# Kernel tuning notes

Hardware: AMD Instinct MI355X
Metric: run time of the kernel (lower is better)

Reference implementation:

```python
import jax, jax.numpy as jnp
import numpy as np


def setup_inputs() -> dict:
    key = jax.random.key(0)
    ks = jax.random.split(key, 12)
    B, S, D = 2, 1024, 1024       # batch, seq_len, hidden
    DF_S, DF_E, E = 2048, 512, 8   # shared ffn, expert ffn, n_experts
    W = 0.02                       # weight init scale
    x = jax.random.normal(ks[0], (B, S, D), jnp.float32)
    router_weight = jax.random.normal(ks[1], (E, D), jnp.float32) * W
    sh_gate_w = jax.random.normal(ks[2], (DF_S, D), jnp.float32) * W
    sh_up_w = jax.random.normal(ks[3], (DF_S, D), jnp.float32) * W
    sh_down_w = jax.random.normal(ks[4], (D, DF_S), jnp.float32) * W
    gate_q = jax.random.randint(ks[5], (E, DF_E, D), -128, 128, jnp.int32)
    up_q = jax.random.randint(ks[6], (E, DF_E, D), -128, 128, jnp.int32)
    down_q = jax.random.randint(ks[7], (E, D, DF_E), -128, 128, jnp.int32)
    gate_s = jax.random.uniform(ks[8], (E, DF_E), jnp.float32) * 0.001
    up_s = jax.random.uniform(ks[9], (E, DF_E), jnp.float32) * 0.001
    down_s = jax.random.uniform(ks[10], (E, D), jnp.float32) * 0.001
    alpha = 0.5 + jax.random.uniform(ks[11], (E,), jnp.float32)  # effective_alpha per expert
    return dict(x=x, router_weight=router_weight, sh_gate_w=sh_gate_w,
                sh_up_w=sh_up_w, sh_down_w=sh_down_w, gate_s=gate_s,
                up_s=up_s, down_s=down_s, alpha=alpha, gate_q=gate_q,
                up_q=up_q, down_q=down_q, top_k=2)


def reference(x, router_weight, sh_gate_w, sh_up_w, sh_down_w,
              gate_s, up_s, down_s, alpha, gate_q, up_q, down_q, top_k):
    B, S, D = x.shape
    T = B * S
    E = router_weight.shape[0]
    xf = x.reshape(T, D).astype(jnp.float32)
    # shared SwiGLU MLP
    shared = (jax.nn.silu(xf @ sh_gate_w.T) * (xf @ sh_up_w.T)) @ sh_down_w.T  # [T, D]
    # router: top-k + softmax over selected logits
    logits = xf @ router_weight.T                                # [T, E]
    k = min(int(top_k), E)
    vals, idx = jax.lax.top_k(logits, k)
    w = jax.nn.softmax(vals, axis=-1)                            # [T, k]
    # scatter routing weights into dense combine matrix [T, E] (topk idx are distinct)
    combine = jnp.zeros((T, E), jnp.float32).at[jnp.arange(T)[:, None], idx].add(w)
    # on-the-fly dequantization: int8-range quants * per-row scale
    gw = gate_q.astype(jnp.float32) * gate_s[..., None]          # [E, DF_E, D]
    uw = up_q.astype(jnp.float32) * up_s[..., None]              # [E, DF_E, D]
    dw = down_q.astype(jnp.float32) * down_s[..., None]          # [E, D, DF_E]
    # expert SwiGLU for every (token, expert) pair, combined by routing weights
    g = jnp.einsum('td,efd->tef', xf, gw)                        # [T, E, DF_E]
    u = jnp.einsum('td,efd->tef', xf, uw)
    eo = jnp.einsum('tef,edf->ted', jax.nn.silu(g) * u, dw)      # [T, E, D]
    delta = eo - shared[:, None, :]                              # expert output minus shared
    mixed = shared + jnp.einsum('te,ted->td', combine * alpha[None, :], delta)
    return mixed.reshape(B, S, D)
```

## Files before the change

kernel.cpp:

```cpp
#include <hip/hip_runtime.h>
#include <math.h>

#define T_TOK 2048
#define D_DIM 1024
#define E_NUM 8
#define DFS   2048
#define DFE   512

#define BK 32

typedef short short8 __attribute__((ext_vector_type(8)));
typedef float floatx4 __attribute__((ext_vector_type(4)));
typedef unsigned short ushort;

__device__ __forceinline__ ushort f2b(float f) {
  union { float f; unsigned u; } v; v.f = f;
  unsigned r = (v.u + 0x7fffu + ((v.u >> 16) & 1u)) >> 16;
  return (ushort)r;
}

__device__ __forceinline__ void gld16(const ushort* g, ushort* l) {
  __builtin_amdgcn_global_load_lds(
      (const __attribute__((address_space(1))) void*)g,
      (__attribute__((address_space(3))) void*)l,
      16, 0, 0);
}

__device__ __forceinline__ float silu_mul(float g, float u) {
  return (g / (1.f + __expf(-g))) * u;
}

__global__ __launch_bounds__(256) void mega_prep(
    const float* __restrict__ x, const float* __restrict__ rw,
    const float* __restrict__ alpha,
    const float* __restrict__ sg, const float* __restrict__ su,
    const float* __restrict__ sd,
    const int* __restrict__ gq, const int* __restrict__ uq,
    const int* __restrict__ dq,
    int* __restrict__ choice, float2* __restrict__ cpair,
    float* __restrict__ csum, ushort* __restrict__ xb,
    ushort* __restrict__ sgb, ushort* __restrict__ subb,
    ushort* __restrict__ sdb,
    ushort* __restrict__ gqb, ushort* __restrict__ uqb,
    ushort* __restrict__ dqb) {
  const int b = blockIdx.x;
  const int tid = threadIdx.x;
  if (b < 512) {
    __shared__ float xs[4 * D_DIM];
    const size_t base = (size_t)b * 4 * D_DIM;
#pragma unroll
    for (int j = 0; j < 4; ++j) {
      const int idx = j * 1024 + tid * 4;
      float4 v = *(const float4*)(x + base + idx);
      *(float4*)&xs[idx] = v;
      union { ushort u[4]; uint2 p; } o;
      o.u[0] = f2b(v.x); o.u[1] = f2b(v.y); o.u[2] = f2b(v.z); o.u[3] = f2b(v.w);
      *(uint2*)(xb + base + idx) = o.p;
    }
    __syncthreads();
    const int w = tid >> 6, l = tid & 63;
    const int t = b * 4 + w;
    const int e = l >> 3, sub = l & 7;
    const float* wr = rw + e * D_DIM;
    float acc = 0.f;
#pragma unroll
    for (int k = 0; k < 32; ++k) {
      const int d = k * 32 + sub * 4;
      float4 xv = *(const float4*)&xs[w * D_DIM + d];
      float4 wv = *(const float4*)(wr + d);
      acc += xv.x * wv.x + xv.y * wv.y + xv.z * wv.z + xv.w * wv.w;
    }
    acc += __shfl_xor(acc, 1);
    acc += __shfl_xor(acc, 2);
    acc += __shfl_xor(acc, 4);
    float lg[8];
#pragma unroll
    for (int i = 0; i < 8; ++i) lg[i] = __shfl(acc, i * 8);
    if (l == 0) {
      int i0 = 0; float v0 = lg[0];
#pragma unroll
      for (int i = 1; i < E_NUM; ++i) if (lg[i] > v0) { v0 = lg[i]; i0 = i; }
      int i1 = -1; float v1 = -1e30f;
#pragma unroll
      for (int i = 0; i < E_NUM; ++i) {
        if (i == i0) continue;
        if (lg[i] > v1) { v1 = lg[i]; i1 = i; }
      }
      float w0 = 1.f / (1.f + __expf(v1 - v0));
      float w1 = 1.f - w0;
      float c0 = w0 * alpha[i0];
      float c1 = w1 * alpha[i1];
      csum[t] = c0 + c1;
      choice[t] = i0 | (i1 << 4);
      cpair[t] = make_float2(c0, c1);
    }
  } else if (b < 512 + 3072) {
    const int bb = b - 512;
    const int which = bb >> 10;
    const float* src; ushort* dst;
    if (which == 0) { src = sg; dst = sgb; }
    else if (which == 1) { src = su; dst = subb; }
    else { src = sd; dst = sdb; }
    const size_t i = (size_t)(bb & 1023) * 256 + tid;
    const float4* sp = (const float4*)src;
    float4 a = sp[2 * i], c = sp[2 * i + 1];
    union { ushort u[8]; uint4 v; } o;
    o.u[0] = f2b(a.x); o.u[1] = f2b(a.y); o.u[2] = f2b(a.z); o.u[3] = f2b(a.w);
    o.u[4] = f2b(c.x); o.u[5] = f2b(c.y); o.u[6] = f2b(c.z); o.u[7] = f2b(c.w);
    ((uint4*)dst)[i] = o.v;
  } else {
    const int bb = b - 3584;
    const int which = bb >> 11;
    const int* src; ushort* dst;
    if (which == 0) { src = gq; dst = gqb; }
    else if (which == 1) { src = uq; dst = uqb; }
    else { src = dq; dst = dqb; }
    const size_t i = (size_t)(bb & 2047) * 256 + tid;
    const int4* sp = (const int4*)src;
    int4 a = sp[2 * i], c = sp[2 * i + 1];
    union { ushort u[8]; uint4 v; } o;
    o.u[0] = f2b((float)a.x); o.u[1] = f2b((float)a.y);
    o.u[2] = f2b((float)a.z); o.u[3] = f2b((float)a.w);
    o.u[4] = f2b((float)c.x); o.u[5] = f2b((float)c.y);
    o.u[6] = f2b((float)c.z); o.u[7] = f2b((float)c.w);
    ((uint4*)dst)[i] = o.v;
  }
}

__global__ __launch_bounds__(1024) void build_lists(
    const int* __restrict__ choice, int* __restrict__ cnt,
    int* __restrict__ tok_list, uint2* __restrict__ ass) {
  __shared__ int lcnt[E_NUM];
  __shared__ int lbase[E_NUM];
  const int tid = threadIdx.x;
  if (tid < E_NUM) lcnt[tid] = 0;
  __syncthreads();
  uint2 tmp[T_TOK / 1024];
#pragma unroll
  for (int r = 0; r < T_TOK / 1024; ++r) {
    const int t = r * 1024 + tid;
    const int ch = choice[t];
    const int i0 = ch & 15, i1 = ch >> 4;
    const int p0 = atomicAdd(&lcnt[i0], 1);
    tok_list[i0 * T_TOK + p0] = t;
    const int p1 = atomicAdd(&lcnt[i1], 1);
    tok_list[i1 * T_TOK + p1] = t;
    tmp[r] = make_uint2((unsigned)((i0 << 16) | p0), (unsigned)((i1 << 16) | p1));
  }
  __syncthreads();
  if (tid < E_NUM) {
    int b = 0;
    for (int i = 0; i < tid; ++i) b += lcnt[i];
    lbase[tid] = b;
    cnt[tid] = lcnt[tid];
    cnt[8 + tid] = b;
  }
  __syncthreads();
#pragma unroll
  for (int r = 0; r < T_TOK / 1024; ++r) {
    const int t = r * 1024 + tid;
    const uint2 v = tmp[r];
    ass[t] = make_uint2(lbase[v.x >> 16] + (v.x & 0xffffu),
                        lbase[v.y >> 16] + (v.y & 0xffffu));
  }
}

#define SZGU (256 * BK)

__global__ __launch_bounds__(256) void mfma_gateup_all(
    const ushort* __restrict__ xb,
    const ushort* __restrict__ wg, const ushort* __restrict__ wu,
    const ushort* __restrict__ gq, const ushort* __restrict__ uq,
    const float* __restrict__ gate_s, const float* __restrict__ up_s,
    const int* __restrict__ cnt, const int* __restrict__ tok_list,
    ushort* __restrict__ sbuf, ushort* __restrict__ act) {
  const int bid = blockIdx.x;
  const bool is_sh = (bid < 512);
  const int tid = threadIdx.x;
  const int wave = tid >> 6, lane = tid & 63;
  const int wr = wave >> 1, wc = wave & 1;
  const int srow = lane >> 2;
  const int scol = (((lane & 3) ^ ((lane >> 3) & 3)) * 8);
  const int K = D_DIM;

  int m0, n0, e = 0, ce = 0, ebase = 0;
  const ushort *aR0, *aR1, *g0, *u0;
  if (is_sh) {
    n0 = (bid & 31) * 64;
    m0 = (bid >> 5) * 128;
    aR0 = xb + (size_t)(m0 + wave * 16 + srow) * K + scol;
    aR1 = aR0 + (size_t)64 * K;
    g0 = wg + (size_t)(n0 + wave * 16 + srow) * K + scol;
    u0 = wu + (size_t)(n0 + wave * 16 + srow) * K + scol;
  } else {
    const int r = bid - 512;
    e = r >> 7;
    const int rr = r & 127;
    n0 = (rr & 7) * 64;
    m0 = (rr >> 3) * 128;
    ce = cnt[e];
    if (m0 >= ce) return;
    ebase = cnt[8 + e];
    const int r0 = m0 + wave * 16 + srow;
    const int r1 = r0 + 64;
    const int tk0 = (r0 < ce) ? tok_list[e * T_TOK + r0] : 0;
    const int tk1 = (r1 < ce) ? tok_list[e * T_TOK + r1] : 0;
    aR0 = xb + (size_t)tk0 * K + scol;
    aR1 = xb + (size_t)tk1 * K + scol;
    g0 = gq + (size_t)e * DFE * D_DIM + (size_t)(n0 + wave * 16 + srow) * K + scol;
    u0 = uq + (size_t)e * DFE * D_DIM + (size_t)(n0 + wave * 16 + srow) * K + scol;
  }

  __shared__ ushort L[3 * SZGU];
  const int woff = (wave * 16) * BK;

  floatx4 accg[4][2], accu[4][2];
#pragma unroll
  for (int i = 0; i < 4; ++i)
#pragma unroll
    for (int j = 0; j < 2; ++j) { accg[i][j] = (floatx4)(0.f); accu[i][j] = (floatx4)(0.f); }

  const int kc = (((lane >> 4) ^ ((lane >> 1) & 3)) * 8);
  const int rb = lane & 15;
  const ushort* dA = &L[(wr * 64 + rb) * BK + kc];
  const ushort* dG = &L[128 * BK + (wc * 32 + rb) * BK + kc];
  const ushort* dU = &L[192 * BK + (wc * 32 + rb) * BK + kc];

#define STAGE_GU(bu, kk)                                        \
  do {                                                          \
    gld16(aR0 + (kk) * BK, &L[(bu) * SZGU] + woff);             \
    gld16(aR1 + (kk) * BK, &L[(bu) * SZGU] + 64 * BK + woff);   \
    gld16(g0 + (kk) * BK, &L[(bu) * SZGU] + 128 * BK + woff);   \
    gld16(u0 + (kk) * BK, &L[(bu) * SZGU] + 192 * BK + woff);   \
  } while (0)

  const int NK = K / BK;
  STAGE_GU(0, 0);
  STAGE_GU(1, 1);

#pragma unroll
  for (int k = 0; k < NK; ++k) {
    if (k < NK - 1) {
      asm volatile("s_waitcnt vmcnt(4)" ::: "memory");
    } else {
      asm volatile("s_waitcnt vmcnt(0)" ::: "memory");
    }
    __builtin_amdgcn_s_barrier();
    asm volatile("" ::: "memory");
    const int bo = (k % 3) * SZGU;
    short8 af[4], gf[2], uf[2];
#pragma unroll
    for (int mt = 0; mt < 4; ++mt)
      af[mt] = *(const short8*)&dA[bo + mt * 16 * BK];
#pragma unroll
    for (int nt = 0; nt < 2; ++nt) {
      gf[nt] = *(const short8*)&dG[bo + nt * 16 * BK];
      uf[nt] = *(const short8*)&dU[bo + nt * 16 * BK];
    }
    if (k + 2 < NK) STAGE_GU((k + 2) % 3, k + 2);
#pragma unroll
    for (int mt = 0; mt < 4; ++mt)
#pragma unroll
      for (int nt = 0; nt < 2; ++nt) {
        accg[mt][nt] = __builtin_amdgcn_mfma_f32_16x16x32_bf16(af[mt], gf[nt], accg[mt][nt], 0, 0, 0);
        accu[mt][nt] = __builtin_amdgcn_mfma_f32_16x16x32_bf16(af[mt], uf[nt], accu[mt][nt], 0, 0, 0);
      }
    asm volatile("s_waitcnt lgkmcnt(0)" ::: "memory");
  }
#undef STAGE_GU

  if (is_sh) {
#pragma unroll
    for (int mt = 0; mt < 4; ++mt)
#pragma unroll
      for (int nt = 0; nt < 2; ++nt) {
        const int col = n0 + wc * 32 + nt * 16 + rb;
#pragma unroll
        for (int r = 0; r < 4; ++r) {
          const int row = m0 + wr * 64 + mt * 16 + (lane >> 4) * 4 + r;
          float s = silu_mul(accg[mt][nt][r], accu[mt][nt][r]);
          sbuf[(size_t)row * DFS + col] = f2b(s);
        }
      }
  } else {
#pragma unroll
    for (int mt = 0; mt < 4; ++mt)
#pragma unroll
      for (int nt = 0; nt < 2; ++nt) {
        const int col = n0 + wc * 32 + nt * 16 + rb;
        const float gsc = gate_s[e * DFE + col];
        const float usc = up_s[e * DFE + col];
#pragma unroll
        for (int r = 0; r < 4; ++r) {
          const int slot = m0 + wr * 64 + mt * 16 + (lane >> 4) * 4 + r;
          if (slot < ce) {
            float s = silu_mul(accg[mt][nt][r] * gsc, accu[mt][nt][r] * usc);
            act[(size_t)(ebase + slot) * DFE + col] = f2b(s);
          }
        }
      }
  }
}

#define SZDN (256 * BK)

__global__ __launch_bounds__(256) void mfma_down_all(
    const ushort* __restrict__ sb, const ushort* __restrict__ wd,
    const ushort* __restrict__ act, const ushort* __restrict__ dq,
    const float* __restrict__ down_s, const int* __restrict__ cnt,
    float* __restrict__ shd0, float* __restrict__ shd1,
    float* __restrict__ pbuf) {
  const int bid = blockIdx.x;
  const bool is_sh = (bid < 256);
  const int tid = threadIdx.x;
  const int wave = tid >> 6, lane = tid & 63;
  const int wr = wave >> 1, wc = wave & 1;
  const int srow = lane >> 2;
  const int scol = (((lane & 3) ^ ((lane >> 3) & 3)) * 8);

  int m0, n0, e = 0, ce = 0, ebase = 0;
  const ushort *aR0, *aR1, *bR0, *bR1;
  float* dst;
  if (is_sh) {
    const int z = bid >> 7;
    const int rr = bid & 127;
    n0 = (rr & 7) * 128;
    m0 = (rr >> 3) * 128;
    const int kb = z * (DFS / 2);
    dst = z ? shd1 : shd0;
    aR0 = sb + (size_t)(m0 + wave * 16 + srow) * DFS + kb + scol;
    aR1 = aR0 + (size_t)64 * DFS;
    bR0 = wd + (size_t)(n0 + wave * 16 + srow) * DFS + kb + scol;
    bR1 = bR0 + (size_t)64 * DFS;
  } else {
    const int r = bid - 256;
    e = r >> 7;
    const int rr = r & 127;
    n0 = (rr & 7) * 128;
    m0 = (rr >> 3) * 128;
    ce = cnt[e];
    if (m0 >= ce) return;
    ebase = cnt[8 + e];
    dst = pbuf;
    aR0 = act + (size_t)(ebase + m0 + wave * 16 + srow) * DFE + scol;
    aR1 = aR0 + (size_t)64 * DFE;
    bR0 = dq + (size_t)e * D_DIM * DFE + (size_t)(n0 + wave * 16 + srow) * DFE + scol;
    bR1 = bR0 + (size_t)64 * DFE;
  }

  __shared__ ushort L[3 * SZDN];
  const int woff = (wave * 16) * BK;

  floatx4 acc[4][4];
#pragma unroll
  for (int i = 0; i < 4; ++i)
#pragma unroll
    for (int j = 0; j < 4; ++j) acc[i][j] = (floatx4)(0.f);

  const int kc = (((lane >> 4) ^ ((lane >> 1) & 3)) * 8);
  const int rb = lane & 15;
  const ushort* dA = &L[(wr * 64 + rb) * BK + kc];
  const ushort* dB = &L[128 * BK + (wc * 64 + rb) * BK + kc];

#define STAGE_DN(bu, kk)                                        \
  do {                                                          \
    gld16(aR0 + (kk) * BK, &L[(bu) * SZDN] + woff);             \
    gld16(aR1 + (kk) * BK, &L[(bu) * SZDN] + 64 * BK + woff);   \
    gld16(bR0 + (kk) * BK, &L[(bu) * SZDN] + 128 * BK + woff);  \
    gld16(bR1 + (kk) * BK, &L[(bu) * SZDN] + 192 * BK + woff);  \
  } while (0)

#define DOWN_LOOP(NKC)                                                        \
  do {                                                                        \
    STAGE_DN(0, 0);                                                           \
    STAGE_DN(1, 1);                                                           \
    _Pragma("unroll")                                                         \
    for (int k = 0; k < (NKC); ++k) {                                         \
      if (k < (NKC) - 1) {                                                    \
        asm volatile("s_waitcnt vmcnt(4)" ::: "memory");                      \
      } else {                                                                \
        asm volatile("s_waitcnt vmcnt(0)" ::: "memory");                      \
      }                                                                       \
      __builtin_amdgcn_s_barrier();                                           \
      asm volatile("" ::: "memory");                                          \
      const int bo = (k % 3) * SZDN;                                          \
      short8 af[4], bf[4];                                                    \
      _Pragma("unroll")                                                       \
      for (int mt = 0; mt < 4; ++mt)                                          \
        af[mt] = *(const short8*)&dA[bo + mt * 16 * BK];                      \
      _Pragma("unroll")                                                       \
      for (int nt = 0; nt < 4; ++nt)                                          \
        bf[nt] = *(const short8*)&dB[bo + nt * 16 * BK];                      \
      if (k + 2 < (NKC)) STAGE_DN((k + 2) % 3, k + 2);                        \
      _Pragma("unroll")                                                       \
      for (int mt = 0; mt < 4; ++mt)                                          \
        _Pragma("unroll")                                                     \
        for (int nt = 0; nt < 4; ++nt)                                        \
          acc[mt][nt] = __builtin_amdgcn_mfma_f32_16x16x32_bf16(af[mt], bf[nt], acc[mt][nt], 0, 0, 0); \
      asm volatile("s_waitcnt lgkmcnt(0)" ::: "memory");                      \
    }                                                                         \
  } while (0)

  if (is_sh) {
    DOWN_LOOP(DFS / 2 / BK);
  } else {
    DOWN_LOOP(DFE / BK);
  }
#undef DOWN_LOOP
#undef STAGE_DN

  if (is_sh) {
#pragma unroll
    for (int mt = 0; mt < 4; ++mt)
#pragma unroll
      for (int nt = 0; nt < 4; ++nt) {
        const int col = n0 + wc * 64 + nt * 16 + rb;
#pragma unroll
        for (int r = 0; r < 4; ++r) {
          const int row = m0 + wr * 64 + mt * 16 + (lane >> 4) * 4 + r;
          dst[(size_t)row * D_DIM + col] = acc[mt][nt][r];
        }
      }
  } else {
#pragma unroll
    for (int mt = 0; mt < 4; ++mt)
#pragma unroll
      for (int nt = 0; nt < 4; ++nt) {
        const int col = n0 + wc * 64 + nt * 16 + rb;
        const float dsc = down_s[e * D_DIM + col];
#pragma unroll
        for (int r = 0; r < 4; ++r) {
          const int slot = m0 + wr * 64 + mt * 16 + (lane >> 4) * 4 + r;
          if (slot < ce)
            dst[(size_t)(ebase + slot) * D_DIM + col] = acc[mt][nt][r] * dsc;
        }
      }
  }
}

__global__ __launch_bounds__(256) void combine_kernel(
    const float* __restrict__ shd0, const float* __restrict__ shd1,
    const float* __restrict__ pbuf, const float* __restrict__ csum,
    const float2* __restrict__ cpair, const uint2* __restrict__ ass,
    float* __restrict__ out) {
  const int t = blockIdx.x;
  const int c4 = threadIdx.x * 4;
  const float cs = 1.f - csum[t];
  const float2 cp = cpair[t];
  const uint2 a = ass[t];
  const size_t idx = (size_t)t * D_DIM + c4;
  float4 s0 = *(const float4*)(shd0 + idx);
  float4 s1 = *(const float4*)(shd1 + idx);
  float4 e0 = *(const float4*)(pbuf + (size_t)a.x * D_DIM + c4);
  float4 e1 = *(const float4*)(pbuf + (size_t)a.y * D_DIM + c4);
  float4 o;
  o.x = cs * (s0.x + s1.x) + cp.x * e0.x + cp.y * e1.x;
  o.y = cs * (s0.y + s1.y) + cp.x * e0.y + cp.y * e1.y;
  o.z = cs * (s0.z + s1.z) + cp.x * e0.z + cp.y * e1.z;
  o.w = cs * (s0.w + s1.w) + cp.x * e0.w + cp.y * e1.w;
  *(float4*)(out + idx) = o;
}

extern "C" void kernel_launch(void* const* d_in, const int* in_sizes, int n_in,
                              void* d_out, int out_size, void* d_ws, size_t ws_size,
                              hipStream_t stream) {
  const float* x         = (const float*)d_in[0];
  const float* rw        = (const float*)d_in[1];
  const float* sh_gate_w = (const float*)d_in[2];
  const float* sh_up_w   = (const float*)d_in[3];
  const float* sh_down_w = (const float*)d_in[4];
  const float* gate_s    = (const float*)d_in[5];
  const float* up_s      = (const float*)d_in[6];
  const float* down_s    = (const float*)d_in[7];
  const float* alpha     = (const float*)d_in[8];
  const int*   gate_q    = (const int*)d_in[9];
  const int*   up_q      = (const int*)d_in[10];
  const int*   down_q    = (const int*)d_in[11];

  char* ws = (char*)d_ws;
  const size_t MB = 1u << 20;
  int*    cnt      = (int*)ws;
  int*    tok_list = (int*)(ws + 1024);
  float*  csum     = (float*)(ws + 66560);
  int*    choice   = (int*)(ws + 74752);
  float2* cpair    = (float2*)(ws + 82944);
  uint2*  ass      = (uint2*)(ws + 99328);
  ushort* xb      = (ushort*)(ws + 1 * MB);
  ushort* sgb     = (ushort*)(ws + 5 * MB);
  ushort* sub     = (ushort*)(ws + 9 * MB);
  float*  shd0    = (float*)(ws + 5 * MB);
  ushort* sbuf    = (ushort*)(ws + 13 * MB);
  ushort* sdb     = (ushort*)(ws + 21 * MB);
  ushort* gqb     = (ushort*)(ws + 25 * MB);
  ushort* uqb     = (ushort*)(ws + 33 * MB);
  float*  pbuf    = (float*)(ws + 25 * MB);
  ushort* dqb     = (ushort*)(ws + 41 * MB);
  ushort* act     = (ushort*)(ws + 49 * MB);
  float*  shd1    = (float*)(ws + 53 * MB);

  float* out = (float*)d_out;

  mega_prep<<<9728, 256, 0, stream>>>(
      x, rw, alpha, sh_gate_w, sh_up_w, sh_down_w, gate_q, up_q, down_q,
      choice, cpair, csum, xb, sgb, sub, sdb, gqb, uqb, dqb);
  build_lists<<<1, 1024, 0, stream>>>(choice, cnt, tok_list, ass);

  mfma_gateup_all<<<512 + 1024, 256, 0, stream>>>(
      xb, sgb, sub, gqb, uqb, gate_s, up_s, cnt, tok_list, sbuf, act);
  mfma_down_all<<<256 + 1024, 256, 0, stream>>>(
      sbuf, sdb, act, dqb, down_s, cnt, shd0, shd1, pbuf);
  combine_kernel<<<T_TOK, 256, 0, stream>>>(shd0, shd1, pbuf, csum, cpair, ass, out);
}
```

Measured before the change: 219.7 us.

## Fuse combine into down GEMM epilogue via atomics; switch to double buffering

Drops the separate combine kernel. The output is zeroed inside the prep kernel, and the down-projection epilogue atomically adds the weighted shared and expert contributions straight into the output, using per-slot routing weights that build_lists now records. It also cuts the LDS staging pipeline from triple to double buffering, with a full vmcnt(0) wait on every iteration. The aim is to save a kernel launch and the intermediate partial-output buffers, at the cost of heavy scattered float atomics and less load/compute overlap in both GEMMs.

```diff
diff --git a/kernel.cpp b/kernel.cpp
--- a/kernel.cpp
+++ b/kernel.cpp
@@ -42,7 +42,7 @@
     ushort* __restrict__ sgb, ushort* __restrict__ subb,
     ushort* __restrict__ sdb,
     ushort* __restrict__ gqb, ushort* __restrict__ uqb,
-    ushort* __restrict__ dqb) {
+    ushort* __restrict__ dqb, float* __restrict__ outz) {
   const int b = blockIdx.x;
   const int tid = threadIdx.x;
   if (b < 512) {
@@ -108,7 +108,7 @@
     o.u[0] = f2b(a.x); o.u[1] = f2b(a.y); o.u[2] = f2b(a.z); o.u[3] = f2b(a.w);
     o.u[4] = f2b(c.x); o.u[5] = f2b(c.y); o.u[6] = f2b(c.z); o.u[7] = f2b(c.w);
     ((uint4*)dst)[i] = o.v;
-  } else {
+  } else if (b < 512 + 3072 + 6144) {
     const int bb = b - 3584;
     const int which = bb >> 11;
     const int* src; ushort* dst;
@@ -124,44 +124,42 @@
     o.u[4] = f2b((float)c.x); o.u[5] = f2b((float)c.y);
     o.u[6] = f2b((float)c.z); o.u[7] = f2b((float)c.w);
     ((uint4*)dst)[i] = o.v;
+  } else {
+    const int bb = b - 9728;
+    float4* op = (float4*)outz + (size_t)bb * 4096 + tid;
+    const float4 z = make_float4(0.f, 0.f, 0.f, 0.f);
+#pragma unroll
+    for (int i = 0; i < 16; ++i) op[i * 256] = z;
   }
 }
 
 __global__ __launch_bounds__(1024) void build_lists(
-    const int* __restrict__ choice, int* __restrict__ cnt,
-    int* __restrict__ tok_list, uint2* __restrict__ ass) {
+    const int* __restrict__ choice, const float2* __restrict__ cpair,
+    int* __restrict__ cnt, int* __restrict__ tok_list,
+    float* __restrict__ cw) {
   __shared__ int lcnt[E_NUM];
-  __shared__ int lbase[E_NUM];
   const int tid = threadIdx.x;
   if (tid < E_NUM) lcnt[tid] = 0;
   __syncthreads();
-  uint2 tmp[T_TOK / 1024];
 #pragma unroll
   for (int r = 0; r < T_TOK / 1024; ++r) {
     const int t = r * 1024 + tid;
     const int ch = choice[t];
+    const float2 cp = cpair[t];
     const int i0 = ch & 15, i1 = ch >> 4;
     const int p0 = atomicAdd(&lcnt[i0], 1);
     tok_list[i0 * T_TOK + p0] = t;
+    cw[i0 * T_TOK + p0] = cp.x;
     const int p1 = atomicAdd(&lcnt[i1], 1);
     tok_list[i1 * T_TOK + p1] = t;
-    tmp[r] = make_uint2((unsigned)((i0 << 16) | p0), (unsigned)((i1 << 16) | p1));
+    cw[i1 * T_TOK + p1] = cp.y;
   }
   __syncthreads();
   if (tid < E_NUM) {
     int b = 0;
     for (int i = 0; i < tid; ++i) b += lcnt[i];
-    lbase[tid] = b;
     cnt[tid] = lcnt[tid];
     cnt[8 + tid] = b;
-  }
-  __syncthreads();
-#pragma unroll
-  for (int r = 0; r < T_TOK / 1024; ++r) {
-    const int t = r * 1024 + tid;
-    const uint2 v = tmp[r];
-    ass[t] = make_uint2(lbase[v.x >> 16] + (v.x & 0xffffu),
-                        lbase[v.y >> 16] + (v.y & 0xffffu));
   }
 }
 
@@ -211,7 +209,7 @@
     u0 = uq + (size_t)e * DFE * D_DIM + (size_t)(n0 + wave * 16 + srow) * K + scol;
   }
 
-  __shared__ ushort L[3 * SZGU];
+  __shared__ ushort L[2 * SZGU];
   const int woff = (wave * 16) * BK;
 
   floatx4 accg[4][2], accu[4][2];
@@ -236,18 +234,13 @@
 
   const int NK = K / BK;
   STAGE_GU(0, 0);
-  STAGE_GU(1, 1);
 
 #pragma unroll
   for (int k = 0; k < NK; ++k) {
-    if (k < NK - 1) {
-      asm volatile("s_waitcnt vmcnt(4)" ::: "memory");
-    } else {
-      asm volatile("s_waitcnt vmcnt(0)" ::: "memory");
-    }
+    asm volatile("s_waitcnt vmcnt(0)" ::: "memory");
     __builtin_amdgcn_s_barrier();
     asm volatile("" ::: "memory");
-    const int bo = (k % 3) * SZGU;
+    const int bo = (k & 1) * SZGU;
     short8 af[4], gf[2], uf[2];
 #pragma unroll
     for (int mt = 0; mt < 4; ++mt)
@@ -257,7 +250,7 @@
       gf[nt] = *(const short8*)&dG[bo + nt * 16 * BK];
       uf[nt] = *(const short8*)&dU[bo + nt * 16 * BK];
     }
-    if (k + 2 < NK) STAGE_GU((k + 2) % 3, k + 2);
+    if (k + 1 < NK) STAGE_GU((k + 1) & 1, k + 1);
 #pragma unroll
     for (int mt = 0; mt < 4; ++mt)
 #pragma unroll
@@ -308,8 +301,8 @@
     const ushort* __restrict__ sb, const ushort* __restrict__ wd,
     const ushort* __restrict__ act, const ushort* __restrict__ dq,
     const float* __restrict__ down_s, const int* __restrict__ cnt,
-    float* __restrict__ shd0, float* __restrict__ shd1,
-    float* __restrict__ pbuf) {
+    const int* __restrict__ tok_list, const float* __restrict__ cw,
+    const float* __restrict__ csum, float* __restrict__ out) {
   const int bid = blockIdx.x;
   const bool is_sh = (bid < 256);
   const int tid = threadIdx.x;
@@ -320,14 +313,12 @@
 
   int m0, n0, e = 0, ce = 0, ebase = 0;
   const ushort *aR0, *aR1, *bR0, *bR1;
-  float* dst;
   if (is_sh) {
     const int z = bid >> 7;
     const int rr = bid & 127;
     n0 = (rr & 7) * 128;
     m0 = (rr >> 3) * 128;
     const int kb = z * (DFS / 2);
-    dst = z ? shd1 : shd0;
     aR0 = sb + (size_t)(m0 + wave * 16 + srow) * DFS + kb + scol;
     aR1 = aR0 + (size_t)64 * DFS;
     bR0 = wd + (size_t)(n0 + wave * 16 + srow) * DFS + kb + scol;
@@ -341,14 +332,13 @@
     ce = cnt[e];
     if (m0 >= ce) return;
     ebase = cnt[8 + e];
-    dst = pbuf;
     aR0 = act + (size_t)(ebase + m0 + wave * 16 + srow) * DFE + scol;
     aR1 = aR0 + (size_t)64 * DFE;
     bR0 = dq + (size_t)e * D_DIM * DFE + (size_t)(n0 + wave * 16 + srow) * DFE + scol;
     bR1 = bR0 + (size_t)64 * DFE;
   }
 
-  __shared__ ushort L[3 * SZDN];
+  __shared__ ushort L[2 * SZDN];
   const int woff = (wave * 16) * BK;
 
   floatx4 acc[4][4];
@@ -373,17 +363,12 @@
 #define DOWN_LOOP(NKC)                                                        \
   do {                                                                        \
     STAGE_DN(0, 0);                                                           \
-    STAGE_DN(1, 1);                                                           \
     _Pragma("unroll")                                                         \
     for (int k = 0; k < (NKC); ++k) {                                         \
-      if (k < (NKC) - 1) {                                                    \
-        asm volatile("s_waitcnt vmcnt(4)" ::: "memory");                      \
-      } else {                                                                \
-        asm volatile("s_waitcnt vmcnt(0)" ::: "memory");                      \
-      }                                                                       \
+      asm volatile("s_waitcnt vmcnt(0)" ::: "memory");                        \
       __builtin_amdgcn_s_barrier();                                           \
       asm volatile("" ::: "memory");                                          \
-      const int bo = (k % 3) * SZDN;                                          \
+      const int bo = (k & 1) * SZDN;                                          \
       short8 af[4], bf[4];                                                    \
       _Pragma("unroll")                                                       \
       for (int mt = 0; mt < 4; ++mt)                                          \
@@ -391,7 +376,7 @@
       _Pragma("unroll")                                                       \
       for (int nt = 0; nt < 4; ++nt)                                          \
         bf[nt] = *(const short8*)&dB[bo + nt * 16 * BK];                      \
-      if (k + 2 < (NKC)) STAGE_DN((k + 2) % 3, k + 2);                        \
+      if (k + 1 < (NKC)) STAGE_DN((k + 1) & 1, k + 1);                        \
       _Pragma("unroll")                                                       \
       for (int mt = 0; mt < 4; ++mt)                                          \
         _Pragma("unroll")                                                     \
@@ -418,7 +403,8 @@
 #pragma unroll
         for (int r = 0; r < 4; ++r) {
           const int row = m0 + wr * 64 + mt * 16 + (lane >> 4) * 4 + r;
-          dst[(size_t)row * D_DIM + col] = acc[mt][nt][r];
+          const float w = 1.f - csum[row];
+          atomicAdd(&out[(size_t)row * D_DIM + col], w * acc[mt][nt][r]);
         }
       }
   } else {
@@ -431,34 +417,14 @@
 #pragma unroll
         for (int r = 0; r < 4; ++r) {
           const int slot = m0 + wr * 64 + mt * 16 + (lane >> 4) * 4 + r;
-          if (slot < ce)
-            dst[(size_t)(ebase + slot) * D_DIM + col] = acc[mt][nt][r] * dsc;
+          if (slot < ce) {
+            const int tk = tok_list[e * T_TOK + slot];
+            const float w = cw[e * T_TOK + slot];
+            atomicAdd(&out[(size_t)tk * D_DIM + col], w * dsc * acc[mt][nt][r]);
+          }
         }
       }
   }
-}
-
-__global__ __launch_bounds__(256) void combine_kernel(
-    const float* __restrict__ shd0, const float* __restrict__ shd1,
-    const float* __restrict__ pbuf, const float* __restrict__ csum,
-    const float2* __restrict__ cpair, const uint2* __restrict__ ass,
-    float* __restrict__ out) {
-  const int t = blockIdx.x;
-  const int c4 = threadIdx.x * 4;
-  const float cs = 1.f - csum[t];
-  const float2 cp = cpair[t];
-  const uint2 a = ass[t];
-  const size_t idx = (size_t)t * D_DIM + c4;
-  float4 s0 = *(const float4*)(shd0 + idx);
-  float4 s1 = *(const float4*)(shd1 + idx);
-  float4 e0 = *(const float4*)(pbuf + (size_t)a.x * D_DIM + c4);
-  float4 e1 = *(const float4*)(pbuf + (size_t)a.y * D_DIM + c4);
-  float4 o;
-  o.x = cs * (s0.x + s1.x) + cp.x * e0.x + cp.y * e1.x;
-  o.y = cs * (s0.y + s1.y) + cp.x * e0.y + cp.y * e1.y;
-  o.z = cs * (s0.z + s1.z) + cp.x * e0.z + cp.y * e1.z;
-  o.w = cs * (s0.w + s1.w) + cp.x * e0.w + cp.y * e1.w;
-  *(float4*)(out + idx) = o;
 }
 
 extern "C" void kernel_launch(void* const* d_in, const int* in_sizes, int n_in,
@@ -484,30 +450,26 @@
   float*  csum     = (float*)(ws + 66560);
   int*    choice   = (int*)(ws + 74752);
   float2* cpair    = (float2*)(ws + 82944);
-  uint2*  ass      = (uint2*)(ws + 99328);
+  float*  cw       = (float*)(ws + 115712);
   ushort* xb      = (ushort*)(ws + 1 * MB);
   ushort* sgb     = (ushort*)(ws + 5 * MB);
   ushort* sub     = (ushort*)(ws + 9 * MB);
-  float*  shd0    = (float*)(ws + 5 * MB);
   ushort* sbuf    = (ushort*)(ws + 13 * MB);
   ushort* sdb     = (ushort*)(ws + 21 * MB);
   ushort* gqb     = (ushort*)(ws + 25 * MB);
   ushort* uqb     = (ushort*)(ws + 33 * MB);
-  float*  pbuf    = (float*)(ws + 25 * MB);
   ushort* dqb     = (ushort*)(ws + 41 * MB);
   ushort* act     = (ushort*)(ws + 49 * MB);
-  float*  shd1    = (float*)(ws + 53 * MB);
 
   float* out = (float*)d_out;
 
-  mega_prep<<<9728, 256, 0, stream>>>(
+  mega_prep<<<9856, 256, 0, stream>>>(
       x, rw, alpha, sh_gate_w, sh_up_w, sh_down_w, gate_q, up_q, down_q,
-      choice, cpair, csum, xb, sgb, sub, sdb, gqb, uqb, dqb);
-  build_lists<<<1, 1024, 0, stream>>>(choice, cnt, tok_list, ass);
+      choice, cpair, csum, xb, sgb, sub, sdb, gqb, uqb, dqb, out);
+  build_lists<<<1, 1024, 0, stream>>>(choice, cpair, cnt, tok_list, cw);
 
   mfma_gateup_all<<<512 + 1024, 256, 0, stream>>>(
       xb, sgb, sub, gqb, uqb, gate_s, up_s, cnt, tok_list, sbuf, act);
   mfma_down_all<<<256 + 1024, 256, 0, stream>>>(
-      sbuf, sdb, act, dqb, down_s, cnt, shd0, shd1, pbuf);
-  combine_kernel<<<T_TOK, 256, 0, stream>>>(shd0, shd1, pbuf, csum, cpair, ass, out);
-}
+      sbuf, sdb, act, dqb, down_s, cnt, tok_list, cw, csum, out);
+}
```

Result: slower. 244.2 us (+11.2%).
